# Optimization experiments

Measured on AMD Instinct MI355X. Metric: run time of the kernel, lower is better.

The kernel has to match this reference:

```python
import jax, jax.numpy as jnp
import numpy as np

THRESHOLD = 1.0
NEG_SLOPE = 0.2
N_NODES = 100000
N_EDGES = 1600000
DIM = 64
N_LAYERS = 3


def setup_inputs() -> dict:
    key = jax.random.key(0)
    ks = jax.random.split(key, 6)
    x = jax.random.normal(ks[0], (N_NODES, DIM), dtype=jnp.float32)
    edge_index = jax.random.randint(ks[1], (2, N_EDGES), 0, N_NODES, dtype=jnp.int64)
    scale = 1.0 / np.sqrt(DIM)
    W = jax.random.normal(ks[2], (N_LAYERS, DIM, DIM), dtype=jnp.float32) * scale
    a_src = jax.random.normal(ks[3], (N_LAYERS, DIM), dtype=jnp.float32) * scale
    a_dst = jax.random.normal(ks[4], (N_LAYERS, DIM), dtype=jnp.float32) * scale
    b = jnp.zeros((N_LAYERS, DIM), dtype=jnp.float32)
    return {"x": x, "edge_index": edge_index, "W": W, "a_src": a_src, "a_dst": a_dst, "b": b}


def reference(x, edge_index, W, a_src, a_dst, b):
    N = x.shape[0]
    # GATConv default add_self_loops=True: append (i -> i) for every node
    self_loop = jnp.arange(N, dtype=edge_index.dtype)
    src = jnp.concatenate([edge_index[0], self_loop])  # message source j
    dst = jnp.concatenate([edge_index[1], self_loop])  # message target i

    h = x
    for l in range(W.shape[0]):
        hw = h @ W[l]                       # [N, d] linear transform
        alpha_s = hw @ a_src[l]             # [N] per-node src attention logits
        alpha_d = hw @ a_dst[l]             # [N] per-node dst attention logits
        e = jax.nn.leaky_relu(alpha_s[src] + alpha_d[dst], NEG_SLOPE)  # [E']
        # softmax over incoming edges of each dst node (segment softmax)
        m = jax.ops.segment_max(e, dst, num_segments=N)
        p = jnp.exp(e - m[dst])
        s = jax.ops.segment_sum(p, dst, num_segments=N)
        attn = p / s[dst]
        out = jax.ops.segment_sum(attn[:, None] * hw[src], dst, num_segments=N)
        h = jnp.clip(out + b[l], -THRESHOLD, THRESHOLD)  # act_fn = clamp
    return h
```

## Files before the change

### kernel.cpp

```cpp
#include <hip/hip_runtime.h>
#include <hip/hip_fp16.h>

#define NN 100000
#define NE 1600000
#define DIM 64
#define NL 3
#define SLOPE 0.2f

#define BSH 9
#define NBUCK ((NN + 511) >> BSH)
#define EPT 16
#define TILE (256 * EPT)
#define MT 128

static __device__ __forceinline__ float lrelu(float x) { return x > 0.f ? x : SLOPE * x; }

static __device__ __forceinline__ float4 load_h4(const ushort* __restrict__ base, size_t off) {
    uint2 u = *(const uint2*)(base + off);
    __half2 h0 = __builtin_bit_cast(__half2, u.x);
    __half2 h1 = __builtin_bit_cast(__half2, u.y);
    float2 f0 = __half22float2(h0);
    float2 f1 = __half22float2(h1);
    return make_float4(f0.x, f0.y, f1.x, f1.y);
}


__global__ __launch_bounds__(256) void k_bucket_hist(const int* __restrict__ ei, int* __restrict__ bcnt) {
    __shared__ int h[256];
    int t = threadIdx.x;
    h[t] = 0;
    __syncthreads();
    for (int e = blockIdx.x * 256 + t; e < NE; e += 256 * 256) atomicAdd(&h[ei[NE + e] >> BSH], 1);
    __syncthreads();
    if (t < NBUCK && h[t]) atomicAdd(&bcnt[t], h[t]);
}

__global__ void k_bucket_scan(const int* __restrict__ bcnt, int* __restrict__ bbase, int* __restrict__ bcur,
                              int* __restrict__ offs) {
    __shared__ int sm[256];
    int t = threadIdx.x;
    sm[t] = (t < NBUCK) ? bcnt[t] : 0;
    __syncthreads();
    for (int off = 1; off < 256; off <<= 1) {
        int x = (t >= off) ? sm[t - off] : 0;
        __syncthreads();
        sm[t] += x;
        __syncthreads();
    }
    if (t < NBUCK) {
        int ex = (t == 0) ? 0 : sm[t - 1];
        bbase[t] = ex;
        bcur[t] = ex;
    }
    if (t == 0) {
        bbase[NBUCK] = NE;
        offs[NN] = NE;
    }
}

__global__ __launch_bounds__(256) void k_partition(const int* __restrict__ ei, int* __restrict__ bcur,
                                                   int2* __restrict__ pairs) {
    __shared__ int2 tile[TILE];
    __shared__ int cnt[256], ofsx[256], gdel[256], sm[256];
    int t = threadIdx.x;
    int ts = blockIdx.x * TILE;
    int tilecnt = NE - ts;
    if (tilecnt > TILE) tilecnt = TILE;
    cnt[t] = 0;
    __syncthreads();
    int srcv[EPT], dstv[EPT], rk[EPT];
#pragma unroll
    for (int k = 0; k < EPT; k++) {
        int e = ts + k * 256 + t;
        if (e < NE) {
            srcv[k] = ei[e];
            dstv[k] = ei[NE + e];
            rk[k] = atomicAdd(&cnt[dstv[k] >> BSH], 1);
        } else {
            rk[k] = -1;
        }
    }
    __syncthreads();
    sm[t] = cnt[t];
    __syncthreads();
    for (int off = 1; off < 256; off <<= 1) {
        int x = (t >= off) ? sm[t - off] : 0;
        __syncthreads();
        sm[t] += x;
        __syncthreads();
    }
    ofsx[t] = (t == 0) ? 0 : sm[t - 1];
    __syncthreads();
#pragma unroll
    for (int k = 0; k < EPT; k++) {
        if (rk[k] >= 0) tile[ofsx[dstv[k] >> BSH] + rk[k]] = make_int2(srcv[k], dstv[k]);
    }
    if (t < NBUCK && cnt[t]) gdel[t] = atomicAdd(&bcur[t], cnt[t]) - ofsx[t];
    __syncthreads();
    for (int i = t; i < tilecnt; i += 256) {
        int2 p = tile[i];
        pairs[gdel[p.y >> BSH] + i] = p;
    }
}

__global__ __launch_bounds__(256) void k_node_csr(const int2* __restrict__ pairs, const int* __restrict__ bbase,
                                                  int* __restrict__ offs, int* __restrict__ csr) {
    __shared__ int deg[512], sofs[512], scur[512], sm[256];
    int t = threadIdx.x;
    int b = blockIdx.x;
    int nodeBase = b << BSH;
    int nNodes = NN - nodeBase;
    if (nNodes > 512) nNodes = 512;
    deg[t] = 0;
    deg[t + 256] = 0;
    __syncthreads();
    int ebeg = bbase[b], eend = bbase[b + 1];
    for (int i = ebeg + t; i < eend; i += 256) atomicAdd(&deg[pairs[i].y - nodeBase], 1);
    __syncthreads();
    int a0 = deg[2 * t], a1 = deg[2 * t + 1];
    sm[t] = a0 + a1;
    __syncthreads();
    for (int off = 1; off < 256; off <<= 1) {
        int x = (t >= off) ? sm[t - off] : 0;
        __syncthreads();
        sm[t] += x;
        __syncthreads();
    }
    int base = (t == 0) ? 0 : sm[t - 1];
    sofs[2 * t] = base;
    sofs[2 * t + 1] = base + a0;
    scur[2 * t] = 0;
    scur[2 * t + 1] = 0;
    __syncthreads();
    for (int n = t; n < nNodes; n += 256) offs[nodeBase + n] = ebeg + sofs[n];
    for (int i = ebeg + t; i < eend; i += 256) {
        int2 p = pairs[i];
        int ln = p.y - nodeBase;
        int r = atomicAdd(&scur[ln], 1);
        csr[ebeg + sofs[ln] + r] = p.x;
    }
}


__global__ __launch_bounds__(256) void k_transform(const float* __restrict__ h, const float* __restrict__ W,
                                                   const float* __restrict__ avs, const float* __restrict__ avd,
                                                   ushort* __restrict__ hw, float* __restrict__ als,
                                                   float* __restrict__ ald) {
    __shared__ float sh[MT][65];
    __shared__ float sw[64][64];
    int t = threadIdx.x;
    int tx = t & 15, ty = t >> 4;
    int base = blockIdx.x * MT;
    int rows = NN - base;
    if (rows > MT) rows = MT;
    {
        const float4* Wv = (const float4*)W;
        float4* swv = (float4*)sw;
        for (int i = t; i < 1024; i += 256) swv[i] = Wv[i];
    }
    for (int i = t; i < MT * 16; i += 256) {
        int r = i >> 4, cs = i & 15;
        float4 v = (r < rows) ? *(const float4*)(h + (size_t)(base + r) * 64 + cs * 4)
                              : make_float4(0.f, 0.f, 0.f, 0.f);
        sh[r][cs * 4 + 0] = v.x;
        sh[r][cs * 4 + 1] = v.y;
        sh[r][cs * 4 + 2] = v.z;
        sh[r][cs * 4 + 3] = v.w;
    }
    __syncthreads();
    float acc[8][4] = {};
    int r0 = ty * 8;
#pragma unroll 4
    for (int k = 0; k < 64; k++) {
        float4 b = *(const float4*)(&sw[k][tx * 4]);
#pragma unroll
        for (int r = 0; r < 8; r++) {
            float a = sh[r0 + r][k];
            acc[r][0] = fmaf(a, b.x, acc[r][0]);
            acc[r][1] = fmaf(a, b.y, acc[r][1]);
            acc[r][2] = fmaf(a, b.z, acc[r][2]);
            acc[r][3] = fmaf(a, b.w, acc[r][3]);
        }
    }
    float4 as4 = *(const float4*)(avs + tx * 4);
    float4 ad4 = *(const float4*)(avd + tx * 4);
#pragma unroll
    for (int r = 0; r < 8; r++) {
        int row = r0 + r;
        bool ok = row < rows;
        if (ok) {
            __half2 h0 = __floats2half2_rn(acc[r][0], acc[r][1]);
            __half2 h1 = __floats2half2_rn(acc[r][2], acc[r][3]);
            uint2 u;
            u.x = __builtin_bit_cast(unsigned int, h0);
            u.y = __builtin_bit_cast(unsigned int, h1);
            *(uint2*)(hw + (size_t)(base + row) * 64 + tx * 4) = u;
        }
        float ps = acc[r][0] * as4.x + acc[r][1] * as4.y + acc[r][2] * as4.z + acc[r][3] * as4.w;
        float pd = acc[r][0] * ad4.x + acc[r][1] * ad4.y + acc[r][2] * ad4.z + acc[r][3] * ad4.w;
#pragma unroll
        for (int off = 1; off <= 8; off <<= 1) {
            ps += __shfl_xor(ps, off);
            pd += __shfl_xor(pd, off);
        }
        if (tx == 0 && ok) {
            als[base + row] = ps;
            ald[base + row] = pd;
        }
    }
}

__global__ __launch_bounds__(256) void k_aggregate(const ushort* __restrict__ hw, const float* __restrict__ als,
                                                   const float* __restrict__ ald, const int* __restrict__ offs,
                                                   const int* __restrict__ csr, const float* __restrict__ bv,
                                                   float* __restrict__ out) {
    int t = threadIdx.x, wave = t >> 6, lane = t & 63;
    int i = blockIdx.x * 4 + wave;
    if (i >= NN) return;
    int q = lane >> 4, c = lane & 15;
    float ad = ald[i];
    float eself = lrelu(als[i] + ad);
    float m = eself;
    float s = 0.f;
    float4 acc = make_float4(0.f, 0.f, 0.f, 0.f);
    int beg = offs[i], end = offs[i + 1];
    for (int cb = beg; cb < end; cb += 64) {
        int cnt = end - cb;
        if (cnt > 64) cnt = 64;
        int src = 0;
        float e = -1e30f;
        if (lane < cnt) {
            src = csr[cb + lane];
            e = lrelu(als[src] + ad);
        }
        float cm = e;
#pragma unroll
        for (int off = 32; off; off >>= 1) cm = fmaxf(cm, __shfl_xor(cm, off));
        float mn = fmaxf(m, cm);
        float p = (lane < cnt) ? __expf(e - mn) : 0.f;
        float cs = p;
#pragma unroll
        for (int off = 32; off; off >>= 1) cs += __shfl_xor(cs, off);
        float sc = __expf(m - mn);
        s = fmaf(s, sc, cs);
        acc.x *= sc;
        acc.y *= sc;
        acc.z *= sc;
        acc.w *= sc;
        m = mn;
        int steps = (cnt + 15) >> 4;
        for (int st = 0; st < steps; st++) {
            int jb = st * 16 + q;
            int s0 = __shfl(src, jb);
            int s1 = __shfl(src, jb + 4);
            int s2 = __shfl(src, jb + 8);
            int s3 = __shfl(src, jb + 12);
            float p0 = __shfl(p, jb);
            float p1 = __shfl(p, jb + 4);
            float p2 = __shfl(p, jb + 8);
            float p3 = __shfl(p, jb + 12);
            float4 v0 = load_h4(hw, (size_t)s0 * 64 + c * 4);
            float4 v1 = load_h4(hw, (size_t)s1 * 64 + c * 4);
            float4 v2 = load_h4(hw, (size_t)s2 * 64 + c * 4);
            float4 v3 = load_h4(hw, (size_t)s3 * 64 + c * 4);
            acc.x = fmaf(p0, v0.x, acc.x);
            acc.y = fmaf(p0, v0.y, acc.y);
            acc.z = fmaf(p0, v0.z, acc.z);
            acc.w = fmaf(p0, v0.w, acc.w);
            acc.x = fmaf(p1, v1.x, acc.x);
            acc.y = fmaf(p1, v1.y, acc.y);
            acc.z = fmaf(p1, v1.z, acc.z);
            acc.w = fmaf(p1, v1.w, acc.w);
            acc.x = fmaf(p2, v2.x, acc.x);
            acc.y = fmaf(p2, v2.y, acc.y);
            acc.z = fmaf(p2, v2.z, acc.z);
            acc.w = fmaf(p2, v2.w, acc.w);
            acc.x = fmaf(p3, v3.x, acc.x);
            acc.y = fmaf(p3, v3.y, acc.y);
            acc.z = fmaf(p3, v3.z, acc.z);
            acc.w = fmaf(p3, v3.w, acc.w);
        }
    }
#pragma unroll
    for (int off = 16; off <= 32; off <<= 1) {
        acc.x += __shfl_xor(acc.x, off);
        acc.y += __shfl_xor(acc.y, off);
        acc.z += __shfl_xor(acc.z, off);
        acc.w += __shfl_xor(acc.w, off);
    }
    float ps = __expf(eself - m);
    s += ps;
    float4 hv = load_h4(hw, (size_t)i * 64 + c * 4);
    acc.x = fmaf(ps, hv.x, acc.x);
    acc.y = fmaf(ps, hv.y, acc.y);
    acc.z = fmaf(ps, hv.z, acc.z);
    acc.w = fmaf(ps, hv.w, acc.w);
    float inv = 1.f / s;
    const float4 bq = *(const float4*)(bv + c * 4);
    float4 o;
    o.x = fminf(fmaxf(fmaf(acc.x, inv, bq.x), -1.f), 1.f);
    o.y = fminf(fmaxf(fmaf(acc.y, inv, bq.y), -1.f), 1.f);
    o.z = fminf(fmaxf(fmaf(acc.z, inv, bq.z), -1.f), 1.f);
    o.w = fminf(fmaxf(fmaf(acc.w, inv, bq.w), -1.f), 1.f);
    if (q == 0) *(float4*)(out + (size_t)i * 64 + c * 4) = o;
}


extern "C" void kernel_launch(void* const* d_in, const int* in_sizes, int n_in, void* d_out, int out_size,
                              void* d_ws, size_t ws_size, hipStream_t stream) {
    const float* x = (const float*)d_in[0];
    const int* ei = (const int*)d_in[1];
    const float* W = (const float*)d_in[2];
    const float* a_s = (const float*)d_in[3];
    const float* a_d = (const float*)d_in[4];
    const float* b = (const float*)d_in[5];
    float* out = (float*)d_out;

    char* w = (char*)d_ws;
    auto alloc = [&](size_t bytes) -> char* {
        char* p = w;
        w += (bytes + 255) & ~(size_t)255;
        return p;
    };
    int* bcnt = (int*)alloc(256 * 4);
    int* bbase = (int*)alloc(257 * 4);
    int* bcur = (int*)alloc(256 * 4);
    int* offs = (int*)alloc((NN + 1) * 4);
    int* csr = (int*)alloc((size_t)NE * 4);
    size_t layer_bytes = (size_t)(2 * NN) * 4 + (size_t)NN * DIM * 2;
    size_t build_bytes = (size_t)NE * 8;
    char* region = alloc(layer_bytes > build_bytes ? layer_bytes : build_bytes);
    int2* pairs = (int2*)region;
    float* als = (float*)region;
    float* ald = als + NN;
    ushort* hwb = (ushort*)(ald + NN);

    hipMemsetAsync(bcnt, 0, 256 * 4, stream);
    k_bucket_hist<<<256, 256, 0, stream>>>(ei, bcnt);
    k_bucket_scan<<<1, 256, 0, stream>>>(bcnt, bbase, bcur, offs);
    k_partition<<<(NE + TILE - 1) / TILE, 256, 0, stream>>>(ei, bcur, pairs);
    k_node_csr<<<NBUCK, 256, 0, stream>>>(pairs, bbase, offs, csr);

    const float* hin = x;
    for (int l = 0; l < NL; l++) {
        k_transform<<<(NN + MT - 1) / MT, 256, 0, stream>>>(hin, W + l * DIM * DIM, a_s + l * DIM, a_d + l * DIM,
                                                            hwb, als, ald);
        k_aggregate<<<(NN + 3) / 4, 256, 0, stream>>>(hwb, als, ald, offs, csr, b + l * DIM, out);
        hin = out;
    }
}
```

Baseline: 357.8 us.

## Map one node per 16-lane group in aggregate and vectorize edge loads in CSR build

The aggregate kernel now assigns each 16-lane group its own destination node instead of one node per 64-lane wave. Edge chunks shrink to 16, and the cross-group accumulator reduction is removed. With about 17 edges per node, this is meant to cut wasted lanes and shuffles in the softmax reductions and allow more gathers in flight. In exchange, lanes within a wave now diverge on differing node degrees. The histogram and partition kernels also load edge indices with int4 vector reads, and partition gets a fast path for full tiles, which changes the edge order within a tile.

Measured after the change: 338.8 us. -5.3%, faster.

```diff
diff --git a/kernel.cpp b/kernel.cpp
--- a/kernel.cpp
+++ b/kernel.cpp
@@ -30,7 +30,15 @@
     int t = threadIdx.x;
     h[t] = 0;
     __syncthreads();
-    for (int e = blockIdx.x * 256 + t; e < NE; e += 256 * 256) atomicAdd(&h[ei[NE + e] >> BSH], 1);
+    const int4* d4 = (const int4*)(ei + NE);
+    int idx = blockIdx.x * 256 + t;
+    if (idx < NE / 4) {
+        int4 v = d4[idx];
+        atomicAdd(&h[v.x >> BSH], 1);
+        atomicAdd(&h[v.y >> BSH], 1);
+        atomicAdd(&h[v.z >> BSH], 1);
+        atomicAdd(&h[v.w >> BSH], 1);
+    }
     __syncthreads();
     if (t < NBUCK && h[t]) atomicAdd(&bcnt[t], h[t]);
 }
@@ -69,15 +77,34 @@
     cnt[t] = 0;
     __syncthreads();
     int srcv[EPT], dstv[EPT], rk[EPT];
-#pragma unroll
-    for (int k = 0; k < EPT; k++) {
-        int e = ts + k * 256 + t;
-        if (e < NE) {
-            srcv[k] = ei[e];
-            dstv[k] = ei[NE + e];
-            rk[k] = atomicAdd(&cnt[dstv[k] >> BSH], 1);
-        } else {
-            rk[k] = -1;
+    int ebase = ts + t * EPT;
+    if (ts + TILE <= NE) {
+#pragma unroll
+        for (int j = 0; j < EPT / 4; j++) {
+            int4 sv = *(const int4*)(ei + ebase + j * 4);
+            int4 dv = *(const int4*)(ei + NE + ebase + j * 4);
+            srcv[j * 4 + 0] = sv.x;
+            srcv[j * 4 + 1] = sv.y;
+            srcv[j * 4 + 2] = sv.z;
+            srcv[j * 4 + 3] = sv.w;
+            dstv[j * 4 + 0] = dv.x;
+            dstv[j * 4 + 1] = dv.y;
+            dstv[j * 4 + 2] = dv.z;
+            dstv[j * 4 + 3] = dv.w;
+        }
+#pragma unroll
+        for (int k = 0; k < EPT; k++) rk[k] = atomicAdd(&cnt[dstv[k] >> BSH], 1);
+    } else {
+#pragma unroll
+        for (int k = 0; k < EPT; k++) {
+            int e = ebase + k;
+            if (e < NE) {
+                srcv[k] = ei[e];
+                dstv[k] = ei[NE + e];
+                rk[k] = atomicAdd(&cnt[dstv[k] >> BSH], 1);
+            } else {
+                rk[k] = -1;
+            }
         }
     }
     __syncthreads();
@@ -91,9 +118,13 @@
     }
     ofsx[t] = (t == 0) ? 0 : sm[t - 1];
     __syncthreads();
-#pragma unroll
-    for (int k = 0; k < EPT; k++) {
-        if (rk[k] >= 0) tile[ofsx[dstv[k] >> BSH] + rk[k]] = make_int2(srcv[k], dstv[k]);
+    if (ts + TILE <= NE) {
+#pragma unroll
+        for (int k = 0; k < EPT; k++) tile[ofsx[dstv[k] >> BSH] + rk[k]] = make_int2(srcv[k], dstv[k]);
+    } else {
+#pragma unroll
+        for (int k = 0; k < EPT; k++)
+            if (rk[k] >= 0) tile[ofsx[dstv[k] >> BSH] + rk[k]] = make_int2(srcv[k], dstv[k]);
     }
     if (t < NBUCK && cnt[t]) gdel[t] = atomicAdd(&bcur[t], cnt[t]) - ofsx[t];
     __syncthreads();
@@ -215,32 +246,33 @@
                                                    const int* __restrict__ csr, const float* __restrict__ bv,
                                                    float* __restrict__ out) {
     int t = threadIdx.x, wave = t >> 6, lane = t & 63;
-    int i = blockIdx.x * 4 + wave;
+    int grp = lane >> 4, l = lane & 15;
+    int grpbase = grp << 4;
+    int i = blockIdx.x * 16 + wave * 4 + grp;
     if (i >= NN) return;
-    int q = lane >> 4, c = lane & 15;
     float ad = ald[i];
     float eself = lrelu(als[i] + ad);
     float m = eself;
     float s = 0.f;
     float4 acc = make_float4(0.f, 0.f, 0.f, 0.f);
     int beg = offs[i], end = offs[i + 1];
-    for (int cb = beg; cb < end; cb += 64) {
+    for (int cb = beg; cb < end; cb += 16) {
         int cnt = end - cb;
-        if (cnt > 64) cnt = 64;
+        if (cnt > 16) cnt = 16;
         int src = 0;
         float e = -1e30f;
-        if (lane < cnt) {
-            src = csr[cb + lane];
+        if (l < cnt) {
+            src = csr[cb + l];
             e = lrelu(als[src] + ad);
         }
         float cm = e;
 #pragma unroll
-        for (int off = 32; off; off >>= 1) cm = fmaxf(cm, __shfl_xor(cm, off));
+        for (int off = 1; off <= 8; off <<= 1) cm = fmaxf(cm, __shfl_xor(cm, off));
         float mn = fmaxf(m, cm);
-        float p = (lane < cnt) ? __expf(e - mn) : 0.f;
+        float p = (l < cnt) ? __expf(e - mn) : 0.f;
         float cs = p;
 #pragma unroll
-        for (int off = 32; off; off >>= 1) cs += __shfl_xor(cs, off);
+        for (int off = 1; off <= 8; off <<= 1) cs += __shfl_xor(cs, off);
         float sc = __expf(m - mn);
         s = fmaf(s, sc, cs);
         acc.x *= sc;
@@ -248,21 +280,21 @@
         acc.z *= sc;
         acc.w *= sc;
         m = mn;
-        int steps = (cnt + 15) >> 4;
-        for (int st = 0; st < steps; st++) {
-            int jb = st * 16 + q;
+        int iters = (cnt + 3) >> 2;
+        for (int j = 0; j < iters; j++) {
+            int jb = grpbase + j * 4;
             int s0 = __shfl(src, jb);
-            int s1 = __shfl(src, jb + 4);
-            int s2 = __shfl(src, jb + 8);
-            int s3 = __shfl(src, jb + 12);
+            int s1 = __shfl(src, jb + 1);
+            int s2 = __shfl(src, jb + 2);
+            int s3 = __shfl(src, jb + 3);
             float p0 = __shfl(p, jb);
-            float p1 = __shfl(p, jb + 4);
-            float p2 = __shfl(p, jb + 8);
-            float p3 = __shfl(p, jb + 12);
-            float4 v0 = load_h4(hw, (size_t)s0 * 64 + c * 4);
-            float4 v1 = load_h4(hw, (size_t)s1 * 64 + c * 4);
-            float4 v2 = load_h4(hw, (size_t)s2 * 64 + c * 4);
-            float4 v3 = load_h4(hw, (size_t)s3 * 64 + c * 4);
+            float p1 = __shfl(p, jb + 1);
+            float p2 = __shfl(p, jb + 2);
+            float p3 = __shfl(p, jb + 3);
+            float4 v0 = load_h4(hw, (size_t)s0 * 64 + l * 4);
+            float4 v1 = load_h4(hw, (size_t)s1 * 64 + l * 4);
+            float4 v2 = load_h4(hw, (size_t)s2 * 64 + l * 4);
+            float4 v3 = load_h4(hw, (size_t)s3 * 64 + l * 4);
             acc.x = fmaf(p0, v0.x, acc.x);
             acc.y = fmaf(p0, v0.y, acc.y);
             acc.z = fmaf(p0, v0.z, acc.z);
@@ -281,28 +313,21 @@
             acc.w = fmaf(p3, v3.w, acc.w);
         }
     }
-#pragma unroll
-    for (int off = 16; off <= 32; off <<= 1) {
-        acc.x += __shfl_xor(acc.x, off);
-        acc.y += __shfl_xor(acc.y, off);
-        acc.z += __shfl_xor(acc.z, off);
-        acc.w += __shfl_xor(acc.w, off);
-    }
     float ps = __expf(eself - m);
     s += ps;
-    float4 hv = load_h4(hw, (size_t)i * 64 + c * 4);
+    float4 hv = load_h4(hw, (size_t)i * 64 + l * 4);
     acc.x = fmaf(ps, hv.x, acc.x);
     acc.y = fmaf(ps, hv.y, acc.y);
     acc.z = fmaf(ps, hv.z, acc.z);
     acc.w = fmaf(ps, hv.w, acc.w);
     float inv = 1.f / s;
-    const float4 bq = *(const float4*)(bv + c * 4);
+    const float4 bq = *(const float4*)(bv + l * 4);
     float4 o;
     o.x = fminf(fmaxf(fmaf(acc.x, inv, bq.x), -1.f), 1.f);
     o.y = fminf(fmaxf(fmaf(acc.y, inv, bq.y), -1.f), 1.f);
     o.z = fminf(fmaxf(fmaf(acc.z, inv, bq.z), -1.f), 1.f);
     o.w = fminf(fmaxf(fmaf(acc.w, inv, bq.w), -1.f), 1.f);
-    if (q == 0) *(float4*)(out + (size_t)i * 64 + c * 4) = o;
+    *(float4*)(out + (size_t)i * 64 + l * 4) = o;
 }
 
 
@@ -336,7 +361,7 @@
     ushort* hwb = (ushort*)(ald + NN);
 
     hipMemsetAsync(bcnt, 0, 256 * 4, stream);
-    k_bucket_hist<<<256, 256, 0, stream>>>(ei, bcnt);
+    k_bucket_hist<<<(NE / 4 + 255) / 256, 256, 0, stream>>>(ei, bcnt);
     k_bucket_scan<<<1, 256, 0, stream>>>(bcnt, bbase, bcur, offs);
     k_partition<<<(NE + TILE - 1) / TILE, 256, 0, stream>>>(ei, bcur, pairs);
     k_node_csr<<<NBUCK, 256, 0, stream>>>(pairs, bbase, offs, csr);
@@ -345,7 +370,7 @@
     for (int l = 0; l < NL; l++) {
         k_transform<<<(NN + MT - 1) / MT, 256, 0, stream>>>(hin, W + l * DIM * DIM, a_s + l * DIM, a_d + l * DIM,
                                                             hwb, als, ald);
-        k_aggregate<<<(NN + 3) / 4, 256, 0, stream>>>(hwb, als, ald, offs, csr, b + l * DIM, out);
+        k_aggregate<<<(NN + 15) / 16, 256, 0, stream>>>(hwb, als, ald, offs, csr, b + l * DIM, out);
         hin = out;
     }
 }
```
